# Performance work log

Hardware: AMD Instinct MI355X
Metric: run time of the kernel (lower is better)

The kernel has to match this reference:

```python
import jax, jax.numpy as jnp
import numpy as np

EPS = 1e-7  # Keras backend epsilon


def setup_inputs() -> dict:
    key = jax.random.key(0)
    kx, ka, ke, kp = jax.random.split(key, 4)
    B, N, F, K_, C = 8, 2048, 128, 128, 128
    X = jax.random.normal(kx, (B, N, F), dtype=jnp.float32)
    Au = (jax.random.uniform(ka, (B, N, N)) < 0.05).astype(jnp.float32)
    A = jnp.maximum(Au, jnp.swapaxes(Au, -1, -2))
    W_emb = jax.random.normal(ke, (F, C), dtype=jnp.float32) * 0.1
    W_pool = jax.random.normal(kp, (F, K_), dtype=jnp.float32) * 0.1
    return {"X": X, "A": A, "W_emb": W_emb, "W_pool": W_pool}


def _diffpool(X, A, W_emb, W_pool):
    N = A.shape[-1]
    I = jnp.eye(N, dtype=A.dtype)
    A_ = A + I
    # symmetric normalization D^-1/2 (A+I) D^-1/2
    d = jax.lax.rsqrt(jnp.sum(A_, axis=-1))          # [B, N]
    fltr = A_ * d[..., :, None] * d[..., None, :]    # [B, N, N]

    Z = jnp.einsum('bnm,bmc->bnc', fltr, X @ W_emb)  # embedding GNN (no activation)
    S = jax.nn.softmax(jnp.einsum('bnm,bmk->bnk', fltr, X @ W_pool), axis=-1)  # [B, N, k]

    # link prediction loss: ||A - S S^T||_F per graph, mean over batch
    S_gram = jnp.einsum('bnk,bmk->bnm', S, S)
    LP_loss = jnp.mean(jnp.linalg.norm(A - S_gram, ord='fro', axis=(-1, -2)))

    # entropy loss on assignments
    entr = -jnp.sum(S * jnp.log(S + EPS), axis=-1)   # [B, N]
    entr_loss = jnp.mean(entr)

    X_pooled = jnp.einsum('bnk,bnc->bkc', S, Z)                  # S^T Z
    A_pooled = jnp.einsum('bnk,bnm,bml->bkl', S, A, S)           # S^T A S
    return X_pooled, A_pooled, S, LP_loss, entr_loss


def reference(X, A, W_emb, W_pool):
    return _diffpool(X, A, W_emb, W_pool)
```

## Files before the change

kernel.cpp:

```cpp
#include <hip/hip_runtime.h>
#include <math.h>

typedef __bf16 bf16x8 __attribute__((ext_vector_type(8)));
typedef float  f32x4  __attribute__((ext_vector_type(4)));
typedef unsigned short u16x4 __attribute__((ext_vector_type(4)));

#define DEVI __device__ __forceinline__

static constexpr int NB  = 8;
static constexpr int NN  = 2048;
static constexpr int NF  = 128;
static constexpr int NC2 = 256;
static constexpr int NSK = 16;

static constexpr int OUT_X0  = 0;
static constexpr int OUT_A0  = NB * 128 * 128;
static constexpr int OUT_S0  = OUT_A0 + NB * 128 * 128;
static constexpr int OUT_LP  = OUT_S0 + NB * NN * 128;
static constexpr int OUT_ENT = OUT_LP + 1;

DEVI unsigned short f2b(float f) {
  unsigned int u = __builtin_bit_cast(unsigned int, f);
  u += 0x7fffu + ((u >> 16) & 1u);
  return (unsigned short)(u >> 16);
}
DEVI float b2f(unsigned short h) {
  unsigned int u = ((unsigned int)h) << 16;
  return __builtin_bit_cast(float, u);
}
DEVI void load_lds16(const void* g, void* l) {
  __builtin_amdgcn_global_load_lds(
      (const __attribute__((address_space(1))) void*)g,
      (__attribute__((address_space(3))) void*)l, 16, 0, 0);
}
DEVI int swz(int row) { return (row >> 1) & 3; }

DEVI void stage_a64(const unsigned short* src, int ld, unsigned short* dst,
                    int k0, int tid) {
  const int wave = tid >> 6;
  const int row = tid >> 2, c = tid & 3;
  load_lds16(src + (size_t)row * ld + k0 + ((c ^ swz(row)) << 3), dst + (wave << 9));
}
DEVI void stage_b128(const unsigned short* src, int ld, unsigned short* dst,
                     int k0, int tid) {
  const int wave = tid >> 6;
#pragma unroll
  for (int is = 0; is < 2; ++is) {
    const int row = is * 64 + (tid >> 2);
    const int c   = tid & 3;
    load_lds16(src + (size_t)row * ld + k0 + ((c ^ swz(row)) << 3),
               dst + ((is * 256 + wave * 64) << 3));
  }
}

DEVI void gemm_core64(const unsigned short* Aop, int lda,
                      const unsigned short* Bop, int ldb, int ksteps,
                      unsigned short* lA0, unsigned short* lA1,
                      unsigned short* lB0, unsigned short* lB1,
                      int tid, f32x4 (&acc)[4][2]) {
  const int lane = tid & 63, wave = tid >> 6;
  const int l15 = lane & 15;
  const int sx = (lane >> 4) ^ ((l15 >> 1) & 3);
#pragma unroll
  for (int i = 0; i < 4; ++i) {
    acc[i][0] = (f32x4){0.f, 0.f, 0.f, 0.f};
    acc[i][1] = (f32x4){0.f, 0.f, 0.f, 0.f};
  }
  stage_a64(Aop, lda, lA0, 0, tid);
  stage_b128(Bop, ldb, lB0, 0, tid);
  __syncthreads();
  for (int kt = 0; kt < ksteps; ++kt) {
    unsigned short* curA = (kt & 1) ? lA1 : lA0;
    unsigned short* curB = (kt & 1) ? lB1 : lB0;
    if (kt + 1 < ksteps) {
      const int k0 = (kt + 1) * 32;
      stage_a64(Aop, lda, (kt & 1) ? lA0 : lA1, k0, tid);
      stage_b128(Bop, ldb, (kt & 1) ? lB0 : lB1, k0, tid);
    }
    bf16x8 af[4], bg[2];
#pragma unroll
    for (int i = 0; i < 4; ++i)
      af[i] = *(const bf16x8*)(curA + (((i * 16 + l15) * 4 + sx) << 3));
#pragma unroll
    for (int j = 0; j < 2; ++j)
      bg[j] = *(const bf16x8*)(curB + (((wave * 32 + j * 16 + l15) * 4 + sx) << 3));
#pragma unroll
    for (int i = 0; i < 4; ++i)
#pragma unroll
      for (int j = 0; j < 2; ++j)
        acc[i][j] = __builtin_amdgcn_mfma_f32_16x16x32_bf16(af[i], bg[j],
                                                            acc[i][j], 0, 0, 0);
    __syncthreads();
  }
}

DEVI void gemm_core128(const unsigned short* Aop, int lda,
                       const unsigned short* Bop, int ldb, int ksteps,
                       unsigned short* lA0, unsigned short* lA1,
                       unsigned short* lB0, unsigned short* lB1,
                       int tid, f32x4 (&acc)[4][4]) {
  const int lane = tid & 63, wave = tid >> 6;
  const int wr = wave >> 1, wc = wave & 1;
  const int l15 = lane & 15;
  const int sx = (lane >> 4) ^ ((l15 >> 1) & 3);
#pragma unroll
  for (int i = 0; i < 4; ++i)
#pragma unroll
    for (int j = 0; j < 4; ++j) acc[i][j] = (f32x4){0.f, 0.f, 0.f, 0.f};
  stage_b128(Aop, lda, lA0, 0, tid);
  stage_b128(Bop, ldb, lB0, 0, tid);
  __syncthreads();
  for (int kt = 0; kt < ksteps; ++kt) {
    unsigned short* curA = (kt & 1) ? lA1 : lA0;
    unsigned short* curB = (kt & 1) ? lB1 : lB0;
    if (kt + 1 < ksteps) {
      const int k0 = (kt + 1) * 32;
      stage_b128(Aop, lda, (kt & 1) ? lA0 : lA1, k0, tid);
      stage_b128(Bop, ldb, (kt & 1) ? lB0 : lB1, k0, tid);
    }
    bf16x8 af[4], bg[4];
#pragma unroll
    for (int i = 0; i < 4; ++i)
      af[i] = *(const bf16x8*)(curA + (((wr * 64 + i * 16 + l15) * 4 + sx) << 3));
#pragma unroll
    for (int j = 0; j < 4; ++j)
      bg[j] = *(const bf16x8*)(curB + (((wc * 64 + j * 16 + l15) * 4 + sx) << 3));
#pragma unroll
    for (int i = 0; i < 4; ++i)
#pragma unroll
      for (int j = 0; j < 4; ++j)
        acc[i][j] = __builtin_amdgcn_mfma_f32_16x16x32_bf16(af[i], bg[j],
                                                            acc[i][j], 0, 0, 0);
    __syncthreads();
  }
}

__global__ __launch_bounds__(256) void k_prep(const float* __restrict__ A,
                                              const float* __restrict__ X,
                                              const float* __restrict__ Wemb,
                                              const float* __restrict__ Wpool,
                                              unsigned short* __restrict__ AB,
                                              unsigned short* __restrict__ XB,
                                              unsigned short* __restrict__ WT,
                                              float* __restrict__ dvec,
                                              float* __restrict__ rsum) {
  const int blk = blockIdx.x, tid = threadIdx.x;
  if (blk < 4096) {
    const int row = blk * 4 + (tid >> 6);
    const int lane = tid & 63;
    const f32x4* src = (const f32x4*)(A + ((size_t)row << 11));
    u16x4* dst = (u16x4*)(AB + ((size_t)row << 11));
    float s = 0.f;
#pragma unroll
    for (int it = 0; it < 8; ++it) {
      f32x4 v = src[it * 64 + lane];
      s += v[0] + v[1] + v[2] + v[3];
      u16x4 o;
      o[0] = f2b(v[0]); o[1] = f2b(v[1]); o[2] = f2b(v[2]); o[3] = f2b(v[3]);
      dst[it * 64 + lane] = o;
    }
#pragma unroll
    for (int o2 = 32; o2; o2 >>= 1) s += __shfl_down(s, o2);
    if (lane == 0) { dvec[row] = rsqrtf(s + 1.f); rsum[row] = s; }
  } else if (blk < 4608) {
    const int i0 = (blk - 4096) * 1024 + tid;
    const f32x4* src = (const f32x4*)X;
    u16x4* dst = (u16x4*)XB;
#pragma unroll
    for (int it = 0; it < 4; ++it) {
      f32x4 v = src[i0 + it * 256];
      u16x4 o;
      o[0] = f2b(v[0]); o[1] = f2b(v[1]); o[2] = f2b(v[2]); o[3] = f2b(v[3]);
      dst[i0 + it * 256] = o;
    }
  } else {
    const int e = (blk - 4608) * 256 + tid;
    const int c = e >> 4, f0 = (e & 15) * 8;
    const float* W = (c < 128) ? Wemb : Wpool;
    const int cc = c & 127;
#pragma unroll
    for (int q = 0; q < 8; ++q)
      WT[c * 128 + f0 + q] = f2b(W[(f0 + q) * 128 + cc]);
  }
}

__global__ __launch_bounds__(256) void k_gemm_xw(const unsigned short* __restrict__ XB,
                                                 const unsigned short* __restrict__ WT,
                                                 const float* __restrict__ dvec,
                                                 unsigned short* __restrict__ VT) {
  __shared__ unsigned short lA[2][2048], lB[2][4096];
  const int mt = blockIdx.x, ct = blockIdx.y, tid = threadIdx.x;
  f32x4 acc[4][2];
  gemm_core64(XB + mt * 64 * NF, NF, WT + ct * 128 * NF, NF, NF / 32,
              lA[0], lA[1], lB[0], lB[1], tid, acc);
  const int lane = tid & 63, wave = tid >> 6;
  const int l15 = lane & 15, l4 = (lane >> 4) * 4;
#pragma unroll
  for (int i = 0; i < 4; ++i) {
    const int gr0 = mt * 64 + i * 16 + l4;
    const int b = gr0 >> 11, n0 = gr0 & 2047;
    const f32x4 dv = *(const f32x4*)(dvec + gr0);
#pragma unroll
    for (int j = 0; j < 2; ++j) {
      const int gc = ct * 128 + wave * 32 + j * 16 + l15;
      u16x4 pk;
#pragma unroll
      for (int r = 0; r < 4; ++r) pk[r] = f2b(acc[i][j][r] * dv[r]);
      *(u16x4*)(VT + (((size_t)(b * NC2 + gc)) << 11) + n0) = pk;
    }
  }
}

__global__ __launch_bounds__(256) void k_gemm_nv(const unsigned short* __restrict__ AB,
                                                 const unsigned short* __restrict__ VT,
                                                 const float* __restrict__ dvec,
                                                 unsigned short* __restrict__ YT,
                                                 float* __restrict__ out,
                                                 float* __restrict__ entv) {
  __shared__ unsigned short lA[2][2048], lB[2][4096];
  const int pid = blockIdx.x, tid = threadIdx.x;
  const int b = pid & 7, slot = pid >> 3;
  const int mt = slot >> 1, ct = slot & 1;
  const unsigned short* Aop = AB + ((size_t)b << 22) + (size_t)mt * 64 * NN;
  const unsigned short* Bop = VT + (((size_t)(b * NC2 + ct * 128)) << 11);
  f32x4 acc[4][2];
  gemm_core64(Aop, NN, Bop, NN, NN / 32, lA[0], lA[1], lB[0], lB[1], tid, acc);
  const int lane = tid & 63, wave = tid >> 6;
  const int l15 = lane & 15, l4g = lane >> 4, l4 = l4g * 4;
  f32x4 dv[4];
#pragma unroll
  for (int i = 0; i < 4; ++i)
    dv[i] = *(const f32x4*)(dvec + (b << 11) + mt * 64 + i * 16 + l4);
#pragma unroll
  for (int i = 0; i < 4; ++i) {
    const int n0 = mt * 64 + i * 16 + l4;
#pragma unroll
    for (int j = 0; j < 2; ++j) {
      const int c = ct * 128 + wave * 32 + j * 16 + l15;
      const u16x4 vv = *(const u16x4*)(VT + (((size_t)(b * NC2 + c)) << 11) + n0);
#pragma unroll
      for (int r = 0; r < 4; ++r)
        acc[i][j][r] = (acc[i][j][r] + b2f(vv[r])) * dv[i][r];
    }
  }
  if (ct == 0) {
#pragma unroll
    for (int i = 0; i < 4; ++i) {
      const int n0 = mt * 64 + i * 16 + l4;
#pragma unroll
      for (int j = 0; j < 2; ++j) {
        const int c = wave * 32 + j * 16 + l15;
        u16x4 pk;
#pragma unroll
        for (int r = 0; r < 4; ++r) pk[r] = f2b(acc[i][j][r]);
        *(u16x4*)(YT + (((size_t)(b * 384 + c)) << 11) + n0) = pk;
      }
    }
    return;
  }
  float* mbuf = (float*)lA;
  float* sbuf = mbuf + 256;
  float* tbuf = mbuf + 512;
  float* ebuf = mbuf + 768;
  float rm[4][4], rs[4][4], rt[4][4];
#pragma unroll
  for (int i = 0; i < 4; ++i)
#pragma unroll
    for (int r = 0; r < 4; ++r) {
      float m = fmaxf(acc[i][0][r], acc[i][1][r]);
#pragma unroll
      for (int off = 1; off < 16; off <<= 1) m = fmaxf(m, __shfl_xor(m, off));
      if (l15 == 0) mbuf[wave * 64 + i * 16 + l4 + r] = m;
    }
  __syncthreads();
#pragma unroll
  for (int i = 0; i < 4; ++i)
#pragma unroll
    for (int r = 0; r < 4; ++r) {
      const int row = i * 16 + l4 + r;
      rm[i][r] = fmaxf(fmaxf(mbuf[row], mbuf[64 + row]),
                       fmaxf(mbuf[128 + row], mbuf[192 + row]));
      rs[i][r] = 0.f; rt[i][r] = 0.f;
    }
#pragma unroll
  for (int i = 0; i < 4; ++i)
#pragma unroll
    for (int j = 0; j < 2; ++j)
#pragma unroll
      for (int r = 0; r < 4; ++r) {
        const float xm = acc[i][j][r] - rm[i][r];
        const float e = __expf(xm);
        acc[i][j][r] = e;
        rs[i][r] += e;
        rt[i][r] += xm * e;
      }
#pragma unroll
  for (int i = 0; i < 4; ++i)
#pragma unroll
    for (int r = 0; r < 4; ++r) {
      float s = rs[i][r], t = rt[i][r];
#pragma unroll
      for (int off = 1; off < 16; off <<= 1) {
        s += __shfl_xor(s, off); t += __shfl_xor(t, off);
      }
      if (l15 == 0) {
        sbuf[wave * 64 + i * 16 + l4 + r] = s;
        tbuf[wave * 64 + i * 16 + l4 + r] = t;
      }
    }
  __syncthreads();
  float ent = 0.f;
#pragma unroll
  for (int i = 0; i < 4; ++i)
#pragma unroll
    for (int r = 0; r < 4; ++r) {
      const int row = i * 16 + l4 + r;
      const float s = sbuf[row] + sbuf[64 + row] + sbuf[128 + row] + sbuf[192 + row];
      const float t = tbuf[row] + tbuf[64 + row] + tbuf[128 + row] + tbuf[192 + row];
      const float inv = 1.f / s;
      rs[i][r] = inv;
      ent += __logf(s) - t * inv;
    }
#pragma unroll
  for (int i = 0; i < 4; ++i) {
    const int n0 = mt * 64 + i * 16 + l4;
#pragma unroll
    for (int j = 0; j < 2; ++j) {
      const int c = wave * 32 + j * 16 + l15;
      u16x4 pk;
#pragma unroll
      for (int r = 0; r < 4; ++r) {
        const float sv = acc[i][j][r] * rs[i][r];
        pk[r] = f2b(sv);
        out[OUT_S0 + (((size_t)((b << 11) + n0 + r)) << 7) + c] = sv;
      }
      *(u16x4*)(YT + (((size_t)(b * 384 + 256 + c)) << 11) + n0) = pk;
    }
  }
  if (wave == 0 && l15 == 0) ebuf[l4g] = ent;
  __syncthreads();
  if (tid == 0)
    entv[b * 32 + mt] = ebuf[0] + ebuf[1] + ebuf[2] + ebuf[3];
}

__global__ __launch_bounds__(256) void k_gemm_as(const unsigned short* __restrict__ AB,
                                                 unsigned short* __restrict__ YT) {
  __shared__ unsigned short lA[2][2048], lB[2][4096];
  const int pid = blockIdx.x, tid = threadIdx.x;
  const int b = pid & 7, mt = pid >> 3;
  f32x4 acc[4][2];
  gemm_core64(AB + ((size_t)b << 22) + (size_t)mt * 64 * NN, NN,
              YT + (((size_t)(b * 384 + 256)) << 11), NN, NN / 32,
              lA[0], lA[1], lB[0], lB[1], tid, acc);
  const int lane = tid & 63, wave = tid >> 6;
  const int l15 = lane & 15, l4 = (lane >> 4) * 4;
#pragma unroll
  for (int i = 0; i < 4; ++i) {
    const int n0 = mt * 64 + i * 16 + l4;
#pragma unroll
    for (int j = 0; j < 2; ++j) {
      const int c = wave * 32 + j * 16 + l15;
      u16x4 pk;
#pragma unroll
      for (int r = 0; r < 4; ++r) pk[r] = f2b(acc[i][j][r]);
      *(u16x4*)(YT + (((size_t)(b * 384 + 128 + c)) << 11) + n0) = pk;
    }
  }
}

__global__ __launch_bounds__(256) void k_gemm_p(const unsigned short* __restrict__ YT,
                                                float* __restrict__ Pp) {
  __shared__ unsigned short lA[2][4096], lB[2][4096];
  const int pid = blockIdx.x, tid = threadIdx.x;
  const int b = pid & 7, slot = pid >> 3;
  const int ct = slot % 3, sk = slot / 3;
  f32x4 acc[4][4];
  gemm_core128(YT + (((size_t)(b * 384 + 256)) << 11) + sk * 128, NN,
               YT + (((size_t)(b * 384 + ct * 128)) << 11) + sk * 128, NN, 4,
               lA[0], lA[1], lB[0], lB[1], tid, acc);
  const int lane = tid & 63, wave = tid >> 6;
  const int wr = wave >> 1, wc = wave & 1, l15 = lane & 15, l4 = (lane >> 4) * 4;
  float* dst = Pp + ((size_t)(sk * NB + b)) * 128 * 384;
#pragma unroll
  for (int i = 0; i < 4; ++i) {
    const int p0 = wr * 64 + i * 16 + l4;
#pragma unroll
    for (int j = 0; j < 4; ++j) {
      const int gc = ct * 128 + wc * 64 + j * 16 + l15;
#pragma unroll
      for (int r = 0; r < 4; ++r) dst[(p0 + r) * 384 + gc] = acc[i][j][r];
    }
  }
}

__global__ __launch_bounds__(256) void k_reduce_p(const float* __restrict__ Pp,
                                                  float* __restrict__ trp,
                                                  float* __restrict__ g2p,
                                                  float* __restrict__ out) {
  const int chunk = blockIdx.x, b = blockIdx.y, tid = threadIdx.x;
  const int e = chunk * 256 + tid;
  const int p = e / 384, c = e - p * 384;
  float s = 0.f;
#pragma unroll
  for (int sk = 0; sk < NSK; ++sk)
    s += Pp[((size_t)(sk * NB + b)) * (128 * 384) + e];
  float tr = 0.f, g2 = 0.f;
  if (c < 128) {
    out[OUT_X0 + ((size_t)(b * 128 + p)) * 128 + c] = s;
  } else if (c < 256) {
    out[OUT_A0 + ((size_t)(b * 128 + p)) * 128 + (c - 128)] = s;
    if (c - 128 == p) tr = s;
  } else {
    g2 = s * s;
  }
  __shared__ float rb[512];
  rb[tid] = tr; rb[256 + tid] = g2;
  __syncthreads();
  for (int o = 128; o; o >>= 1) {
    if (tid < o) { rb[tid] += rb[tid + o]; rb[256 + tid] += rb[256 + tid + o]; }
    __syncthreads();
  }
  if (tid == 0) { trp[b * 192 + chunk] = rb[0]; g2p[b * 192 + chunk] = rb[256]; }
}

__global__ __launch_bounds__(256) void k_lp(const float* __restrict__ rsum,
                                            const float* __restrict__ trp,
                                            const float* __restrict__ g2p,
                                            float* __restrict__ lpv) {
  const int b = blockIdx.x, tid = threadIdx.x;
  float nz = 0.f;
#pragma unroll
  for (int i = 0; i < 8; ++i) nz += rsum[(b << 11) + i * 256 + tid];
  float tr = (tid < 192) ? trp[b * 192 + tid] : 0.f;
  float g2 = (tid < 192) ? g2p[b * 192 + tid] : 0.f;
  __shared__ float rb[768];
  rb[tid] = nz; rb[256 + tid] = tr; rb[512 + tid] = g2;
  __syncthreads();
  for (int o = 128; o; o >>= 1) {
    if (tid < o) {
      rb[tid] += rb[tid + o];
      rb[256 + tid] += rb[256 + tid + o];
      rb[512 + tid] += rb[512 + tid + o];
    }
    __syncthreads();
  }
  if (tid == 0)
    lpv[b] = sqrtf(fmaxf(rb[0] - 2.f * rb[256] + rb[512], 0.f));
}

__global__ __launch_bounds__(256) void k_losses(const float* __restrict__ entv,
                                                const float* __restrict__ lpv,
                                                float* __restrict__ out) {
  const int tid = threadIdx.x;
  __shared__ float rb[256];
  rb[tid] = entv[tid];
  __syncthreads();
  for (int o = 128; o; o >>= 1) {
    if (tid < o) rb[tid] += rb[tid + o];
    __syncthreads();
  }
  if (tid == 0) {
    float lp = 0.f;
#pragma unroll
    for (int b = 0; b < 8; ++b) lp += lpv[b];
    out[OUT_LP] = 0.125f * lp;
    out[OUT_ENT] = rb[0] * (1.f / (NB * NN));
  }
}

extern "C" void kernel_launch(void* const* d_in, const int* in_sizes, int n_in,
                              void* d_out, int out_size, void* d_ws, size_t ws_size,
                              hipStream_t stream) {
  const float* X     = (const float*)d_in[0];
  const float* A     = (const float*)d_in[1];
  const float* Wemb  = (const float*)d_in[2];
  const float* Wpool = (const float*)d_in[3];
  float* out = (float*)d_out;

  char* ws = (char*)d_ws;
  size_t o = 0;
  unsigned short* AB = (unsigned short*)(ws + o); o += (size_t)NB * NN * NN * 2;
  unsigned short* XB = (unsigned short*)(ws + o); o += (size_t)NB * NN * NF * 2;
  unsigned short* WT = (unsigned short*)(ws + o); o += (size_t)NC2 * NF * 2;
  unsigned short* VT = (unsigned short*)(ws + o); o += (size_t)NB * NC2 * NN * 2;
  unsigned short* YT = (unsigned short*)(ws + o); o += (size_t)NB * 384 * NN * 2;
  float* Pp  = (float*)(ws + o); o += (size_t)NSK * NB * 128 * 384 * 4;
  float* dvec = (float*)(ws + o); o += (size_t)NB * NN * 4;
  float* rsum = (float*)(ws + o); o += (size_t)NB * NN * 4;
  float* trp  = (float*)(ws + o); o += (size_t)NB * 192 * 4;
  float* g2p  = (float*)(ws + o); o += (size_t)NB * 192 * 4;
  float* entv = (float*)(ws + o); o += 256 * 4;
  float* lpv  = (float*)(ws + o); o += NB * 4;

  k_prep    <<<dim3(4624), 256, 0, stream>>>(A, X, Wemb, Wpool, AB, XB, WT, dvec, rsum);
  k_gemm_xw <<<dim3(NB * NN / 64, 2), 256, 0, stream>>>(XB, WT, dvec, VT);
  k_gemm_nv <<<dim3(512), 256, 0, stream>>>(AB, VT, dvec, YT, out, entv);
  k_gemm_as <<<dim3(256), 256, 0, stream>>>(AB, YT);
  k_gemm_p  <<<dim3(384), 256, 0, stream>>>(YT, Pp);
  k_reduce_p<<<dim3(192, NB), 256, 0, stream>>>(Pp, trp, g2p, out);
  k_lp      <<<dim3(NB), 256, 0, stream>>>(rsum, trp, g2p, lpv);
  k_losses  <<<1, 256, 0, stream>>>(entv, lpv, out);
}
```

Measured before the change: 301.7 us.

## Widen fltr-GEMM tile to all 256 columns so A rows are read once

The k_gemm_nv kernel now computes both the embedding and pooling column halves (256 output columns) in one block instead of splitting them across two blocks. Each adjacency row tile is then streamed from memory once rather than twice, which halves global traffic for A in this GEMM. In exchange, the grid shrinks from 512 to 256 blocks, each with twice the accumulators and a larger LDS footprint. This may reduce occupancy and leave CUs idle on a 256-CU device.

After: 312.7 us. 1.04x slower.

```diff
diff --git a/kernel.cpp b/kernel.cpp
--- a/kernel.cpp
+++ b/kernel.cpp
@@ -46,6 +46,17 @@
   const int wave = tid >> 6;
 #pragma unroll
   for (int is = 0; is < 2; ++is) {
+    const int row = is * 64 + (tid >> 2);
+    const int c   = tid & 3;
+    load_lds16(src + (size_t)row * ld + k0 + ((c ^ swz(row)) << 3),
+               dst + ((is * 256 + wave * 64) << 3));
+  }
+}
+DEVI void stage_b256(const unsigned short* src, int ld, unsigned short* dst,
+                     int k0, int tid) {
+  const int wave = tid >> 6;
+#pragma unroll
+  for (int is = 0; is < 4; ++is) {
     const int row = is * 64 + (tid >> 2);
     const int c   = tid & 3;
     load_lds16(src + (size_t)row * ld + k0 + ((c ^ swz(row)) << 3),
@@ -217,16 +228,51 @@
                                                  unsigned short* __restrict__ YT,
                                                  float* __restrict__ out,
                                                  float* __restrict__ entv) {
-  __shared__ unsigned short lA[2][2048], lB[2][4096];
+  __shared__ __align__(16) unsigned short sm16[20480];
+  float* smf = (float*)sm16;
   const int pid = blockIdx.x, tid = threadIdx.x;
-  const int b = pid & 7, slot = pid >> 3;
-  const int mt = slot >> 1, ct = slot & 1;
+  const int b = pid & 7, mt = pid >> 3;
   const unsigned short* Aop = AB + ((size_t)b << 22) + (size_t)mt * 64 * NN;
-  const unsigned short* Bop = VT + (((size_t)(b * NC2 + ct * 128)) << 11);
-  f32x4 acc[4][2];
-  gemm_core64(Aop, NN, Bop, NN, NN / 32, lA[0], lA[1], lB[0], lB[1], tid, acc);
+  const unsigned short* Bop = VT + (((size_t)(b * NC2)) << 11);
+  unsigned short* lA0 = sm16, *lA1 = sm16 + 2048;
+  unsigned short* lB0 = sm16 + 4096, *lB1 = sm16 + 12288;
   const int lane = tid & 63, wave = tid >> 6;
   const int l15 = lane & 15, l4g = lane >> 4, l4 = l4g * 4;
+  const int sx = (lane >> 4) ^ ((l15 >> 1) & 3);
+  f32x4 acc[4][4];
+#pragma unroll
+  for (int i = 0; i < 4; ++i)
+#pragma unroll
+    for (int j = 0; j < 4; ++j) acc[i][j] = (f32x4){0.f, 0.f, 0.f, 0.f};
+  stage_a64(Aop, NN, lA0, 0, tid);
+  stage_b256(Bop, NN, lB0, 0, tid);
+  __syncthreads();
+  for (int kt = 0; kt < 64; ++kt) {
+    unsigned short* curA = (kt & 1) ? lA1 : lA0;
+    unsigned short* curB = (kt & 1) ? lB1 : lB0;
+    if (kt + 1 < 64) {
+      const int k0 = (kt + 1) * 32;
+      stage_a64(Aop, NN, (kt & 1) ? lA0 : lA1, k0, tid);
+      stage_b256(Bop, NN, (kt & 1) ? lB0 : lB1, k0, tid);
+    }
+    bf16x8 af[4], bg[4];
+#pragma unroll
+    for (int i = 0; i < 4; ++i)
+      af[i] = *(const bf16x8*)(curA + (((i * 16 + l15) * 4 + sx) << 3));
+#pragma unroll
+    for (int j = 0; j < 4; ++j) {
+      const int row = (j < 2) ? (wave * 32 + j * 16 + l15)
+                              : (128 + wave * 32 + (j - 2) * 16 + l15);
+      bg[j] = *(const bf16x8*)(curB + ((row * 4 + sx) << 3));
+    }
+#pragma unroll
+    for (int i = 0; i < 4; ++i)
+#pragma unroll
+      for (int j = 0; j < 4; ++j)
+        acc[i][j] = __builtin_amdgcn_mfma_f32_16x16x32_bf16(af[i], bg[j],
+                                                            acc[i][j], 0, 0, 0);
+    __syncthreads();
+  }
   f32x4 dv[4];
 #pragma unroll
   for (int i = 0; i < 4; ++i)
@@ -235,39 +281,37 @@
   for (int i = 0; i < 4; ++i) {
     const int n0 = mt * 64 + i * 16 + l4;
 #pragma unroll
-    for (int j = 0; j < 2; ++j) {
-      const int c = ct * 128 + wave * 32 + j * 16 + l15;
-      const u16x4 vv = *(const u16x4*)(VT + (((size_t)(b * NC2 + c)) << 11) + n0);
+    for (int j = 0; j < 4; ++j) {
+      const int vrow = (j < 2) ? (wave * 32 + j * 16 + l15)
+                               : (128 + wave * 32 + (j - 2) * 16 + l15);
+      const u16x4 vv = *(const u16x4*)(VT + (((size_t)(b * NC2 + vrow)) << 11) + n0);
 #pragma unroll
       for (int r = 0; r < 4; ++r)
         acc[i][j][r] = (acc[i][j][r] + b2f(vv[r])) * dv[i][r];
     }
   }
-  if (ct == 0) {
-#pragma unroll
-    for (int i = 0; i < 4; ++i) {
-      const int n0 = mt * 64 + i * 16 + l4;
-#pragma unroll
-      for (int j = 0; j < 2; ++j) {
-        const int c = wave * 32 + j * 16 + l15;
-        u16x4 pk;
-#pragma unroll
-        for (int r = 0; r < 4; ++r) pk[r] = f2b(acc[i][j][r]);
-        *(u16x4*)(YT + (((size_t)(b * 384 + c)) << 11) + n0) = pk;
-      }
-    }
-    return;
-  }
-  float* mbuf = (float*)lA;
-  float* sbuf = mbuf + 256;
-  float* tbuf = mbuf + 512;
-  float* ebuf = mbuf + 768;
+#pragma unroll
+  for (int i = 0; i < 4; ++i) {
+    const int n0 = mt * 64 + i * 16 + l4;
+#pragma unroll
+    for (int j = 0; j < 2; ++j) {
+      const int c = wave * 32 + j * 16 + l15;
+      u16x4 pk;
+#pragma unroll
+      for (int r = 0; r < 4; ++r) pk[r] = f2b(acc[i][j][r]);
+      *(u16x4*)(YT + (((size_t)(b * 384 + c)) << 11) + n0) = pk;
+    }
+  }
+  float* mbuf = smf;
+  float* sbuf = smf + 256;
+  float* tbuf = smf + 512;
+  float* ebuf = smf + 768;
   float rm[4][4], rs[4][4], rt[4][4];
 #pragma unroll
   for (int i = 0; i < 4; ++i)
 #pragma unroll
     for (int r = 0; r < 4; ++r) {
-      float m = fmaxf(acc[i][0][r], acc[i][1][r]);
+      float m = fmaxf(acc[i][2][r], acc[i][3][r]);
 #pragma unroll
       for (int off = 1; off < 16; off <<= 1) m = fmaxf(m, __shfl_xor(m, off));
       if (l15 == 0) mbuf[wave * 64 + i * 16 + l4 + r] = m;
@@ -285,7 +329,7 @@
 #pragma unroll
   for (int i = 0; i < 4; ++i)
 #pragma unroll
-    for (int j = 0; j < 2; ++j)
+    for (int j = 2; j < 4; ++j)
 #pragma unroll
       for (int r = 0; r < 4; ++r) {
         const float xm = acc[i][j][r] - rm[i][r];
@@ -325,16 +369,16 @@
   for (int i = 0; i < 4; ++i) {
     const int n0 = mt * 64 + i * 16 + l4;
 #pragma unroll
-    for (int j = 0; j < 2; ++j) {
-      const int c = wave * 32 + j * 16 + l15;
+    for (int j = 2; j < 4; ++j) {
+      const int cs = wave * 32 + (j - 2) * 16 + l15;
       u16x4 pk;
 #pragma unroll
       for (int r = 0; r < 4; ++r) {
         const float sv = acc[i][j][r] * rs[i][r];
         pk[r] = f2b(sv);
-        out[OUT_S0 + (((size_t)((b << 11) + n0 + r)) << 7) + c] = sv;
+        out[OUT_S0 + (((size_t)((b << 11) + n0 + r)) << 7) + cs] = sv;
       }
-      *(u16x4*)(YT + (((size_t)(b * 384 + 256 + c)) << 11) + n0) = pk;
+      *(u16x4*)(YT + (((size_t)(b * 384 + 256 + cs)) << 11) + n0) = pk;
     }
   }
   if (wave == 0 && l15 == 0) ebuf[l4g] = ent;
@@ -494,7 +538,7 @@
 
   k_prep    <<<dim3(4624), 256, 0, stream>>>(A, X, Wemb, Wpool, AB, XB, WT, dvec, rsum);
   k_gemm_xw <<<dim3(NB * NN / 64, 2), 256, 0, stream>>>(XB, WT, dvec, VT);
-  k_gemm_nv <<<dim3(512), 256, 0, stream>>>(AB, VT, dvec, YT, out, entv);
+  k_gemm_nv <<<dim3(256), 256, 0, stream>>>(AB, VT, dvec, YT, out, entv);
   k_gemm_as <<<dim3(256), 256, 0, stream>>>(AB, YT);
   k_gemm_p  <<<dim3(384), 256, 0, stream>>>(YT, Pp);
   k_reduce_p<<<dim3(192, NB), 256, 0, stream>>>(Pp, trp, g2p, out);
```
